# Kernel optimization log

Measured on AMD Instinct MI355X. Metric: run time of the kernel, lower is better.

The kernel has to match this reference:

```python
import jax, jax.numpy as jnp
import numpy as np

N = 50000
DEG = 16
E = N * DEG
IN_F, HID, OUT_F = 512, 128, 64
SLOPE = 0.2


def setup_inputs() -> dict:
    key = jax.random.key(0)
    ks = jax.random.split(key, 10)
    row_ptr = jnp.arange(N + 1, dtype=jnp.int64) * DEG          # uniform-degree CSR
    col_idx = jax.random.randint(ks[0], (E,), 0, N, dtype=jnp.int64)
    x = jax.random.normal(ks[1], (N, IN_F), dtype=jnp.float32)
    s1 = 1.0 / np.sqrt(IN_F)
    s2 = 1.0 / np.sqrt(HID)
    return {
        "row_ptr": row_ptr,
        "col_idx": col_idx,
        "input_feature": x,
        "W1": jax.random.normal(ks[2], (IN_F, HID), dtype=jnp.float32) * s1,
        "attn_l1": jax.random.normal(ks[3], (HID,), dtype=jnp.float32) * s2,
        "attn_r1": jax.random.normal(ks[4], (HID,), dtype=jnp.float32) * s2,
        "bias1": jnp.zeros((HID,), dtype=jnp.float32),
        "W2": jax.random.normal(ks[5], (HID, OUT_F), dtype=jnp.float32) * s2,
        "attn_l2": jax.random.normal(ks[6], (OUT_F,), dtype=jnp.float32) * 0.125,
        "attn_r2": jax.random.normal(ks[7], (OUT_F,), dtype=jnp.float32) * 0.125,
        "bias2": jnp.zeros((OUT_F,), dtype=jnp.float32),
    }


def gat_layer(row_ptr, col_idx, x, W, attn_l, attn_r, bias):
    n = row_ptr.shape[0] - 1
    e = col_idx.shape[0]
    h = x @ W                                   # [N, F] dense GEMM
    el = h @ attn_l                             # [N] dst attention term
    er = h @ attn_r                             # [N] src attention term
    # edge -> destination row via CSR row_ptr
    dst = jnp.searchsorted(row_ptr, jnp.arange(e, dtype=row_ptr.dtype), side="right") - 1
    src = col_idx
    score = jax.nn.leaky_relu(el[dst] + er[src], negative_slope=SLOPE)  # [E]
    # neighborhood softmax over edges sharing a destination
    smax = jax.ops.segment_max(score, dst, num_segments=n)
    ex = jnp.exp(score - smax[dst])
    ssum = jax.ops.segment_sum(ex, dst, num_segments=n)
    alpha = ex / ssum[dst]                      # [E]
    # weighted gather-scatter aggregation
    out = jax.ops.segment_sum(alpha[:, None] * h[src], dst, num_segments=n)
    return out + bias


def reference(row_ptr, col_idx, input_feature, W1, attn_l1, attn_r1, bias1,
              W2, attn_l2, attn_r2, bias2):
    x = gat_layer(row_ptr, col_idx, input_feature, W1, attn_l1, attn_r1, bias1)
    x = gat_layer(row_ptr, col_idx, x, W2, attn_l2, attn_r2, bias2)
    return x
```

## Files before the change

### kernel.cpp

```cpp
#include <hip/hip_runtime.h>
#include <hip/hip_bf16.h>

#define Nn 50000
#define DEG 16
#define IN_F 512
#define HID 128
#define OUT_F 64
#define SLOPE 0.2f

typedef __attribute__((ext_vector_type(8))) short bf16x8;
typedef __attribute__((ext_vector_type(4))) short bf16x4;
typedef __attribute__((ext_vector_type(4))) float f32x4;
typedef __attribute__((ext_vector_type(4))) unsigned int u32x4;

__device__ __forceinline__ unsigned short f2bf(float f) {
    return __builtin_bit_cast(unsigned short, __float2bfloat16(f));
}
__device__ __forceinline__ float bf2f(unsigned short u) {
    return __bfloat162float(__builtin_bit_cast(__hip_bfloat16, u));
}

__global__ void __launch_bounds__(256) prep_kernel(
        const float* __restrict__ W1, const float* __restrict__ W2,
        const int* __restrict__ row_ptr,
        unsigned short* __restrict__ w1t, unsigned short* __restrict__ w2t,
        int* __restrict__ flag64) {
    int g = blockIdx.x * 256 + threadIdx.x;
    if (g == 0) {
        *flag64 = (row_ptr[1] == DEG) ? 0 : 1;
    }
    if (g < HID * IN_F) {
        int c = g >> 9, k = g & 511;
        w1t[g] = f2bf(W1[k * HID + c]);
    } else {
        int g2 = g - HID * IN_F;
        if (g2 < OUT_F * HID) {
            int c = g2 >> 7, k = g2 & 127;
            w2t[g2] = f2bf(W2[k * OUT_F + c]);
        }
    }
}

template<int K, int F, int NWC, int KC, bool A_BF16>
__global__ void __launch_bounds__(256) gemm_fused(
        const void* __restrict__ Ain, const unsigned short* __restrict__ WT,
        const float* __restrict__ alv, const float* __restrict__ arv,
        unsigned short* __restrict__ Hb, float* __restrict__ el,
        float* __restrict__ er, int M) {
    constexpr int NWR = 4 / NWC;
    constexpr int BM  = NWR * 32;
    constexpr int STR = KC + 8;
    constexpr int NCH = K / KC;
    __shared__ unsigned short wt[F * STR];
    __shared__ unsigned short at[BM * STR];
    __shared__ float redl[BM][NWC];
    __shared__ float redr[BM][NWC];

    const int tid  = threadIdx.x;
    const int lane = tid & 63;
    const int w    = tid >> 6;
    const int wr   = w / NWC, wc = w % NWC;
    const int ln   = lane & 15, q = lane >> 4;
    const int mb   = blockIdx.x * BM;

    f32x4 acc[2][4] = {};

    for (int ch = 0; ch < NCH; ++ch) {
        const int k0 = ch * KC;
        constexpr int NCPB = F * KC / 8 / 256;
        #pragma unroll
        for (int i = 0; i < NCPB; ++i) {
            int idx = tid + i * 256;
            int c   = idx / (KC / 8);
            int k8  = (idx % (KC / 8)) * 8;
            *(u32x4*)&wt[c * STR + k8] = *(const u32x4*)&WT[(size_t)c * K + k0 + k8];
        }
        if (A_BF16) {
            const unsigned short* Ab = (const unsigned short*)Ain;
            constexpr int TPR = KC / 8;
            constexpr int RPS = 256 / TPR;
            #pragma unroll
            for (int s = 0; s < BM / RPS; ++s) {
                int row = s * RPS + tid / TPR;
                int k8  = (tid % TPR) * 8;
                int rg  = mb + row; if (rg > M - 1) rg = M - 1;
                *(u32x4*)&at[row * STR + k8] = *(const u32x4*)&Ab[(size_t)rg * K + k0 + k8];
            }
        } else {
            const float* Af = (const float*)Ain;
            constexpr int TPR = KC / 4;
            constexpr int RPS = 256 / TPR;
            #pragma unroll
            for (int s = 0; s < BM / RPS; ++s) {
                int row = s * RPS + tid / TPR;
                int c4  = (tid % TPR) * 4;
                int rg  = mb + row; if (rg > M - 1) rg = M - 1;
                f32x4 v = *(const f32x4*)&Af[(size_t)rg * K + k0 + c4];
                bf16x4 b;
                #pragma unroll
                for (int jj = 0; jj < 4; ++jj) b[jj] = (short)f2bf(v[jj]);
                *(bf16x4*)&at[row * STR + c4] = b;
            }
        }
        __syncthreads();
        #pragma unroll
        for (int ks = 0; ks < KC / 32; ++ks) {
            bf16x8 af0 = *(const bf16x8*)&at[(wr * 32 + ln) * STR + ks * 32 + q * 8];
            bf16x8 af1 = *(const bf16x8*)&at[(wr * 32 + 16 + ln) * STR + ks * 32 + q * 8];
            #pragma unroll
            for (int nt = 0; nt < 4; ++nt) {
                bf16x8 bfr = *(const bf16x8*)&wt[(wc * 64 + nt * 16 + ln) * STR + ks * 32 + q * 8];
                acc[0][nt] = __builtin_amdgcn_mfma_f32_16x16x32_bf16(af0, bfr, acc[0][nt], 0, 0, 0);
                acc[1][nt] = __builtin_amdgcn_mfma_f32_16x16x32_bf16(af1, bfr, acc[1][nt], 0, 0, 0);
            }
        }
        __syncthreads();
    }

    float av[4], bv[4];
    #pragma unroll
    for (int nt = 0; nt < 4; ++nt) {
        av[nt] = alv[wc * 64 + nt * 16 + ln];
        bv[nt] = arv[wc * 64 + nt * 16 + ln];
    }
    #pragma unroll
    for (int fr = 0; fr < 2; ++fr) {
        #pragma unroll
        for (int r = 0; r < 4; ++r) {
            float sl = 0.f, sr = 0.f;
            #pragma unroll
            for (int nt = 0; nt < 4; ++nt) {
                float v = acc[fr][nt][r];
                sl += v * av[nt];
                sr += v * bv[nt];
            }
            #pragma unroll
            for (int m = 1; m < 16; m <<= 1) {
                sl += __shfl_xor(sl, m);
                sr += __shfl_xor(sr, m);
            }
            int rowl = wr * 32 + fr * 16 + q * 4 + r;
            if (ln == 0) { redl[rowl][wc] = sl; redr[rowl][wc] = sr; }
            int grow = mb + rowl;
            if (grow < M) {
                #pragma unroll
                for (int nt = 0; nt < 4; ++nt)
                    Hb[(size_t)grow * F + wc * 64 + nt * 16 + ln] = f2bf(acc[fr][nt][r]);
            }
        }
    }
    __syncthreads();
    if (tid < BM && mb + tid < M) {
        float s1 = redl[tid][0], s2 = redr[tid][0];
        if constexpr (NWC == 2) { s1 += redl[tid][1]; s2 += redr[tid][1]; }
        el[mb + tid] = s1;
        er[mb + tid] = s2;
    }
}

__global__ void __launch_bounds__(256) agg1_k(
        const int* __restrict__ col, const int* __restrict__ flag64,
        const float* __restrict__ el, const float* __restrict__ er,
        const unsigned short* __restrict__ Hb, const float* __restrict__ bias,
        unsigned short* __restrict__ Ob) {
    int lane = threadIdx.x & 63;
    int node = blockIdx.x * 4 + (threadIdx.x >> 6);
    int j    = lane & 15;
    int e    = node * DEG + j;
    int src  = (*flag64) ? (int)((const long long*)col)[e] : col[e];
    float sc = el[node] + er[src];
    sc = sc >= 0.f ? sc : SLOPE * sc;
    float mx = sc;
    #pragma unroll
    for (int m = 1; m < 16; m <<= 1) mx = fmaxf(mx, __shfl_xor(mx, m));
    float ex = __expf(sc - mx);
    float sm = ex;
    #pragma unroll
    for (int m = 1; m < 16; m <<= 1) sm += __shfl_xor(sm, m);
    float alpha = ex / sm;

    float a0 = 0.f, a1 = 0.f;
    #pragma unroll
    for (int jj = 0; jj < DEG; ++jj) {
        int   sj = __shfl(src, jj, 16);
        float aj = __shfl(alpha, jj, 16);
        unsigned int hv = *(const unsigned int*)&Hb[(size_t)sj * HID + lane * 2];
        a0 += aj * bf2f((unsigned short)(hv & 0xffffu));
        a1 += aj * bf2f((unsigned short)(hv >> 16));
    }
    a0 += bias[lane * 2];
    a1 += bias[lane * 2 + 1];
    unsigned int pk = (unsigned int)f2bf(a0) | ((unsigned int)f2bf(a1) << 16);
    *(unsigned int*)&Ob[(size_t)node * HID + lane * 2] = pk;
}

__global__ void __launch_bounds__(256) agg2_k(
        const int* __restrict__ col, const int* __restrict__ flag64,
        const float* __restrict__ el, const float* __restrict__ er,
        const unsigned short* __restrict__ Hb, const float* __restrict__ bias,
        float* __restrict__ out) {
    int lane = threadIdx.x & 63;
    int node = blockIdx.x * 4 + (threadIdx.x >> 6);
    int j    = lane & 15;
    int e    = node * DEG + j;
    int src  = (*flag64) ? (int)((const long long*)col)[e] : col[e];
    float sc = el[node] + er[src];
    sc = sc >= 0.f ? sc : SLOPE * sc;
    float mx = sc;
    #pragma unroll
    for (int m = 1; m < 16; m <<= 1) mx = fmaxf(mx, __shfl_xor(mx, m));
    float ex = __expf(sc - mx);
    float sm = ex;
    #pragma unroll
    for (int m = 1; m < 16; m <<= 1) sm += __shfl_xor(sm, m);
    float alpha = ex / sm;

    float a0 = 0.f;
    #pragma unroll
    for (int jj = 0; jj < DEG; ++jj) {
        int   sj = __shfl(src, jj, 16);
        float aj = __shfl(alpha, jj, 16);
        a0 += aj * bf2f(Hb[(size_t)sj * OUT_F + lane]);
    }
    out[(size_t)node * OUT_F + lane] = a0 + bias[lane];
}

extern "C" void kernel_launch(void* const* d_in, const int* in_sizes, int n_in,
                              void* d_out, int out_size, void* d_ws, size_t ws_size,
                              hipStream_t stream) {
    const int*   row_ptr = (const int*)d_in[0];
    const int*   col_idx = (const int*)d_in[1];
    const float* x   = (const float*)d_in[2];
    const float* W1  = (const float*)d_in[3];
    const float* al1 = (const float*)d_in[4];
    const float* ar1 = (const float*)d_in[5];
    const float* b1  = (const float*)d_in[6];
    const float* W2  = (const float*)d_in[7];
    const float* al2 = (const float*)d_in[8];
    const float* ar2 = (const float*)d_in[9];
    const float* b2  = (const float*)d_in[10];
    float* out = (float*)d_out;

    float* ws = (float*)d_ws;
    unsigned short* h1b = (unsigned short*)ws;
    unsigned short* o1b = (unsigned short*)(ws + 3200000);
    unsigned short* h2b = (unsigned short*)(ws + 6400000);
    float* el1 = ws + 8000000;
    float* er1 = ws + 8050000;
    float* el2 = ws + 8100000;
    float* er2 = ws + 8150000;
    unsigned short* w1t = (unsigned short*)(ws + 8200000);
    unsigned short* w2t = (unsigned short*)(ws + 8232768);
    int* flag64 = (int*)(ws + 8236864);

    prep_kernel<<<(HID * IN_F + OUT_F * HID + 255) / 256, 256, 0, stream>>>(
        W1, W2, row_ptr, w1t, w2t, flag64);

    gemm_fused<512, 128, 2, 128, false><<<(Nn + 63) / 64, 256, 0, stream>>>(
        x, w1t, al1, ar1, h1b, el1, er1, Nn);
    agg1_k<<<Nn / 4, 256, 0, stream>>>(col_idx, flag64, el1, er1, h1b, b1, o1b);

    gemm_fused<128, 64, 1, 128, true><<<(Nn + 127) / 128, 256, 0, stream>>>(
        o1b, w2t, al2, ar2, h2b, el2, er2, Nn);
    agg2_k<<<Nn / 4, 256, 0, stream>>>(col_idx, flag64, el2, er2, h2b, b2, out);
}
```

Before: 270.6 us.

## Replace LDS-staged GEMM with register-direct MFMA loads from global memory

The GEMM kernel no longer stages A and W tiles in shared memory. Each wave loads its A fragments and the transposed-weight fragments straight from global memory into registers, and every wave now covers all F output columns for 32 rows. This removes the LDS copies, the __syncthreads barriers and the cross-wave el/er reduction, since each wave writes its own el/er directly. The trade-off is that each wave re-reads the full weight matrix from global memory or cache instead of sharing it through LDS, and it holds more accumulator registers, which may lower occupancy. The prep kernel's transpose is also rewritten so that it reads W coalesced and writes it scattered.

```diff
diff --git a/kernel.cpp b/kernel.cpp
--- a/kernel.cpp
+++ b/kernel.cpp
@@ -9,9 +9,7 @@
 #define SLOPE 0.2f
 
 typedef __attribute__((ext_vector_type(8))) short bf16x8;
-typedef __attribute__((ext_vector_type(4))) short bf16x4;
 typedef __attribute__((ext_vector_type(4))) float f32x4;
-typedef __attribute__((ext_vector_type(4))) unsigned int u32x4;
 
 __device__ __forceinline__ unsigned short f2bf(float f) {
     return __builtin_bit_cast(unsigned short, __float2bfloat16(f));
@@ -29,99 +27,72 @@
     if (g == 0) {
         *flag64 = (row_ptr[1] == DEG) ? 0 : 1;
     }
-    if (g < HID * IN_F) {
-        int c = g >> 9, k = g & 511;
-        w1t[g] = f2bf(W1[k * HID + c]);
+    if (g < IN_F * HID) {
+        int k = g >> 7, c = g & 127;
+        w1t[c * IN_F + k] = f2bf(W1[g]);
     } else {
-        int g2 = g - HID * IN_F;
-        if (g2 < OUT_F * HID) {
-            int c = g2 >> 7, k = g2 & 127;
-            w2t[g2] = f2bf(W2[k * OUT_F + c]);
-        }
-    }
-}
-
-template<int K, int F, int NWC, int KC, bool A_BF16>
-__global__ void __launch_bounds__(256) gemm_fused(
+        int g2 = g - IN_F * HID;
+        if (g2 < HID * OUT_F) {
+            int k = g2 >> 6, c = g2 & 63;
+            w2t[c * HID + k] = f2bf(W2[g2]);
+        }
+    }
+}
+
+template<int K, int F, bool A_BF16>
+__global__ void __launch_bounds__(256) gemm_reg(
         const void* __restrict__ Ain, const unsigned short* __restrict__ WT,
         const float* __restrict__ alv, const float* __restrict__ arv,
         unsigned short* __restrict__ Hb, float* __restrict__ el,
         float* __restrict__ er, int M) {
-    constexpr int NWR = 4 / NWC;
-    constexpr int BM  = NWR * 32;
-    constexpr int STR = KC + 8;
-    constexpr int NCH = K / KC;
-    __shared__ unsigned short wt[F * STR];
-    __shared__ unsigned short at[BM * STR];
-    __shared__ float redl[BM][NWC];
-    __shared__ float redr[BM][NWC];
-
+    constexpr int NT = F / 16;
     const int tid  = threadIdx.x;
     const int lane = tid & 63;
     const int w    = tid >> 6;
-    const int wr   = w / NWC, wc = w % NWC;
     const int ln   = lane & 15, q = lane >> 4;
-    const int mb   = blockIdx.x * BM;
-
-    f32x4 acc[2][4] = {};
-
-    for (int ch = 0; ch < NCH; ++ch) {
-        const int k0 = ch * KC;
-        constexpr int NCPB = F * KC / 8 / 256;
-        #pragma unroll
-        for (int i = 0; i < NCPB; ++i) {
-            int idx = tid + i * 256;
-            int c   = idx / (KC / 8);
-            int k8  = (idx % (KC / 8)) * 8;
-            *(u32x4*)&wt[c * STR + k8] = *(const u32x4*)&WT[(size_t)c * K + k0 + k8];
-        }
-        if (A_BF16) {
+    const int mb   = blockIdx.x * 128 + w * 32;
+
+    int m0 = mb + ln;      if (m0 > M - 1) m0 = M - 1;
+    int m1 = mb + 16 + ln; if (m1 > M - 1) m1 = M - 1;
+
+    f32x4 acc[2][NT] = {};
+    const unsigned short* bb = WT + (size_t)ln * K;
+
+    #pragma unroll
+    for (int ks = 0; ks < K / 32; ++ks) {
+        const int kk = ks * 32 + q * 8;
+        bf16x8 af0, af1;
+        if constexpr (A_BF16) {
             const unsigned short* Ab = (const unsigned short*)Ain;
-            constexpr int TPR = KC / 8;
-            constexpr int RPS = 256 / TPR;
-            #pragma unroll
-            for (int s = 0; s < BM / RPS; ++s) {
-                int row = s * RPS + tid / TPR;
-                int k8  = (tid % TPR) * 8;
-                int rg  = mb + row; if (rg > M - 1) rg = M - 1;
-                *(u32x4*)&at[row * STR + k8] = *(const u32x4*)&Ab[(size_t)rg * K + k0 + k8];
-            }
+            af0 = *(const bf16x8*)&Ab[(size_t)m0 * K + kk];
+            af1 = *(const bf16x8*)&Ab[(size_t)m1 * K + kk];
         } else {
             const float* Af = (const float*)Ain;
-            constexpr int TPR = KC / 4;
-            constexpr int RPS = 256 / TPR;
+            f32x4 va0 = *(const f32x4*)&Af[(size_t)m0 * K + kk];
+            f32x4 va1 = *(const f32x4*)&Af[(size_t)m0 * K + kk + 4];
+            f32x4 vb0 = *(const f32x4*)&Af[(size_t)m1 * K + kk];
+            f32x4 vb1 = *(const f32x4*)&Af[(size_t)m1 * K + kk + 4];
             #pragma unroll
-            for (int s = 0; s < BM / RPS; ++s) {
-                int row = s * RPS + tid / TPR;
-                int c4  = (tid % TPR) * 4;
-                int rg  = mb + row; if (rg > M - 1) rg = M - 1;
-                f32x4 v = *(const f32x4*)&Af[(size_t)rg * K + k0 + c4];
-                bf16x4 b;
-                #pragma unroll
-                for (int jj = 0; jj < 4; ++jj) b[jj] = (short)f2bf(v[jj]);
-                *(bf16x4*)&at[row * STR + c4] = b;
-            }
-        }
-        __syncthreads();
+            for (int jj = 0; jj < 4; ++jj) {
+                af0[jj]     = (short)f2bf(va0[jj]);
+                af0[jj + 4] = (short)f2bf(va1[jj]);
+                af1[jj]     = (short)f2bf(vb0[jj]);
+                af1[jj + 4] = (short)f2bf(vb1[jj]);
+            }
+        }
         #pragma unroll
-        for (int ks = 0; ks < KC / 32; ++ks) {
-            bf16x8 af0 = *(const bf16x8*)&at[(wr * 32 + ln) * STR + ks * 32 + q * 8];
-            bf16x8 af1 = *(const bf16x8*)&at[(wr * 32 + 16 + ln) * STR + ks * 32 + q * 8];
-            #pragma unroll
-            for (int nt = 0; nt < 4; ++nt) {
-                bf16x8 bfr = *(const bf16x8*)&wt[(wc * 64 + nt * 16 + ln) * STR + ks * 32 + q * 8];
-                acc[0][nt] = __builtin_amdgcn_mfma_f32_16x16x32_bf16(af0, bfr, acc[0][nt], 0, 0, 0);
-                acc[1][nt] = __builtin_amdgcn_mfma_f32_16x16x32_bf16(af1, bfr, acc[1][nt], 0, 0, 0);
-            }
-        }
-        __syncthreads();
-    }
-
-    float av[4], bv[4];
-    #pragma unroll
-    for (int nt = 0; nt < 4; ++nt) {
-        av[nt] = alv[wc * 64 + nt * 16 + ln];
-        bv[nt] = arv[wc * 64 + nt * 16 + ln];
+        for (int nt = 0; nt < NT; ++nt) {
+            bf16x8 bfr = *(const bf16x8*)&bb[(size_t)nt * 16 * K + kk];
+            acc[0][nt] = __builtin_amdgcn_mfma_f32_16x16x32_bf16(af0, bfr, acc[0][nt], 0, 0, 0);
+            acc[1][nt] = __builtin_amdgcn_mfma_f32_16x16x32_bf16(af1, bfr, acc[1][nt], 0, 0, 0);
+        }
+    }
+
+    float av[NT], bv[NT];
+    #pragma unroll
+    for (int nt = 0; nt < NT; ++nt) {
+        av[nt] = alv[nt * 16 + ln];
+        bv[nt] = arv[nt * 16 + ln];
     }
     #pragma unroll
     for (int fr = 0; fr < 2; ++fr) {
@@ -129,7 +100,7 @@
         for (int r = 0; r < 4; ++r) {
             float sl = 0.f, sr = 0.f;
             #pragma unroll
-            for (int nt = 0; nt < 4; ++nt) {
+            for (int nt = 0; nt < NT; ++nt) {
                 float v = acc[fr][nt][r];
                 sl += v * av[nt];
                 sr += v * bv[nt];
@@ -139,22 +110,14 @@
                 sl += __shfl_xor(sl, m);
                 sr += __shfl_xor(sr, m);
             }
-            int rowl = wr * 32 + fr * 16 + q * 4 + r;
-            if (ln == 0) { redl[rowl][wc] = sl; redr[rowl][wc] = sr; }
-            int grow = mb + rowl;
+            int grow = mb + fr * 16 + q * 4 + r;
             if (grow < M) {
                 #pragma unroll
-                for (int nt = 0; nt < 4; ++nt)
-                    Hb[(size_t)grow * F + wc * 64 + nt * 16 + ln] = f2bf(acc[fr][nt][r]);
-            }
-        }
-    }
-    __syncthreads();
-    if (tid < BM && mb + tid < M) {
-        float s1 = redl[tid][0], s2 = redr[tid][0];
-        if constexpr (NWC == 2) { s1 += redl[tid][1]; s2 += redr[tid][1]; }
-        el[mb + tid] = s1;
-        er[mb + tid] = s2;
+                for (int nt = 0; nt < NT; ++nt)
+                    Hb[(size_t)grow * F + nt * 16 + ln] = f2bf(acc[fr][nt][r]);
+                if (ln == 0) { el[grow] = sl; er[grow] = sr; }
+            }
+        }
     }
 }
 
@@ -253,14 +216,14 @@
     unsigned short* w2t = (unsigned short*)(ws + 8232768);
     int* flag64 = (int*)(ws + 8236864);
 
-    prep_kernel<<<(HID * IN_F + OUT_F * HID + 255) / 256, 256, 0, stream>>>(
+    prep_kernel<<<(IN_F * HID + HID * OUT_F + 255) / 256, 256, 0, stream>>>(
         W1, W2, row_ptr, w1t, w2t, flag64);
 
-    gemm_fused<512, 128, 2, 128, false><<<(Nn + 63) / 64, 256, 0, stream>>>(
+    gemm_reg<512, 128, false><<<(Nn + 127) / 128, 256, 0, stream>>>(
         x, w1t, al1, ar1, h1b, el1, er1, Nn);
     agg1_k<<<Nn / 4, 256, 0, stream>>>(col_idx, flag64, el1, er1, h1b, b1, o1b);
 
-    gemm_fused<128, 64, 1, 128, true><<<(Nn + 127) / 128, 256, 0, stream>>>(
+    gemm_reg<128, 64, true><<<(Nn + 127) / 128, 256, 0, stream>>>(
         o1b, w2t, al2, ar2, h2b, el2, er2, Nn);
     agg2_k<<<Nn / 4, 256, 0, stream>>>(col_idx, flag64, el2, er2, h2b, b2, out);
 }
```

After: 256.5 us. -5.2%, faster.
